# Optimization experiments

Measured on AMD Instinct MI355X. Metric: run time of the kernel, lower is better.

The kernel has to match this reference:

```python
import jax, jax.numpy as jnp
import numpy as np

IN, H, B = 1024, 1024, 8192


def _uniform(key, shape, stdv):
    return jax.random.uniform(key, shape, jnp.float32, -stdv, stdv)


def setup_inputs() -> dict:
    key = jax.random.key(0)
    ks = jax.random.split(key, 20)
    stdv = 1.0 / np.sqrt(H)
    inp = {
        "x": jax.random.normal(ks[0], (B, IN), jnp.float32),
        "h": jax.random.normal(ks[1], (B, H), jnp.float32),
        "c": jax.random.normal(ks[2], (B, H), jnp.float32),
        # fused input->gates weight [IN, 4H] (gate order: I, F, G, O) and bias [4H]
        "Wi": _uniform(ks[3], (IN, 4 * H), stdv),
        "bi": _uniform(ks[4], (4 * H,), stdv),
        # fused hidden->gates weight [H, 4H] and bias [4H]
        "Wh": _uniform(ks[5], (H, 4 * H), stdv),
        "bh": _uniform(ks[6], (4 * H,), stdv),
    }
    return inp


def reference(x, h, c, Wi, bi, Wh, bh):
    # Two fused GEMMs replacing the 8 separate nn.Linear calls (same math).
    gates = x @ Wi + bi + h @ Wh + bh  # [B, 4H]
    gI, gF, gG, gO = jnp.split(gates, 4, axis=-1)
    I = jax.nn.sigmoid(gI)
    F = jax.nn.sigmoid(gF)
    G = jnp.tanh(gG)   # nlF = Tanh
    O = jax.nn.sigmoid(gO)
    c_ = F * c + I * G
    h_ = O * jnp.tanh(c_)  # nlF2 = Tanh
    return (h_, c_)
```

## Files before the change

kernel.cpp:

```cpp
#include <hip/hip_runtime.h>
#include <stdint.h>

#define IN_DIM 1024
#define H_DIM  1024
#define BATCH  8192
#define KDIM   2048
#define NDIM   4096
#define BM     256
#define BN     256
#define BK     64
#define NT     (KDIM / BK)

typedef __bf16 bf16x8 __attribute__((ext_vector_type(8)));
typedef float  f32x4  __attribute__((ext_vector_type(4)));
typedef unsigned int u32;

static __device__ __forceinline__ unsigned short f2bf(float f) {
  u32 u = __builtin_bit_cast(u32, f);
  u += 0x7FFFu + ((u >> 16) & 1u);
  return (unsigned short)(u >> 16);
}

static __device__ __forceinline__ float sigm(float x) {
  return 1.0f / (1.0f + __expf(-x));
}
static __device__ __forceinline__ float tanh_fast(float x) {
  float e = __expf(-2.0f * fabsf(x));
  float t = (1.0f - e) / (1.0f + e);
  return copysignf(t, x);
}

__global__ void conv_a(const float* __restrict__ x, const float* __restrict__ h,
                       unsigned short* __restrict__ A) {
  const int total = BATCH * KDIM / 4;
  for (int i = blockIdx.x * blockDim.x + threadIdx.x; i < total;
       i += gridDim.x * blockDim.x) {
    int b = i >> 9;
    int k = (i & 511) << 2;
    const float* src = (k < IN_DIM) ? (x + (size_t)b * IN_DIM + k)
                                    : (h + (size_t)b * H_DIM + (k - IN_DIM));
    float4 v = *reinterpret_cast<const float4*>(src);
    ushort4 o;
    o.x = f2bf(v.x); o.y = f2bf(v.y); o.z = f2bf(v.z); o.w = f2bf(v.w);
    *reinterpret_cast<ushort4*>(A + (size_t)b * KDIM + k) = o;
  }
}

__global__ void conv_b(const float* __restrict__ Wi, const float* __restrict__ Wh,
                       unsigned short* __restrict__ Bt) {
  __shared__ float tile[32][33];
  int k0 = blockIdx.x * 32;
  int c0 = blockIdx.y * 32;
  int tx = threadIdx.x;
  int ty = threadIdx.y;
  const float* src = (k0 < IN_DIM) ? (Wi + (size_t)k0 * NDIM)
                                   : (Wh + (size_t)(k0 - IN_DIM) * NDIM);
  for (int i = 0; i < 4; i++) {
    int r = ty + 8 * i;
    tile[r][tx] = src[(size_t)r * NDIM + c0 + tx];
  }
  __syncthreads();
  int g = c0 >> 10;
  int ubase = c0 & 1023;
  for (int i = 0; i < 4; i++) {
    int cc = ty + 8 * i;
    int u = ubase + cc;
    int j = ((u >> 4) << 6) + (g << 4) + (u & 15);
    Bt[(size_t)j * KDIM + k0 + tx] = f2bf(tile[tx][cc]);
  }
}

__global__ void conv_bias(const float* __restrict__ bi, const float* __restrict__ bh,
                          float* __restrict__ bias) {
  int j = blockIdx.x * blockDim.x + threadIdx.x;
  if (j < NDIM) {
    int u = ((j >> 6) << 4) + (j & 15);
    int g = (j >> 4) & 3;
    int c = (g << 10) + u;
    bias[j] = bi[c] + bh[c];
  }
}

static __device__ __forceinline__ void gload_lds16(const void* g, void* l) {
  __builtin_amdgcn_global_load_lds(
      (const __attribute__((address_space(1))) u32*)g,
      (__attribute__((address_space(3))) u32*)l, 16, 0, 0);
}

#define MFMA __builtin_amdgcn_mfma_f32_16x16x32_bf16
#define SGB  __builtin_amdgcn_sched_group_barrier

__launch_bounds__(512, 2)
__global__ void lstm_gemm(const unsigned short* __restrict__ A,
                          const unsigned short* __restrict__ Bt,
                          const float* __restrict__ bias,
                          const float* __restrict__ Cin,
                          float* __restrict__ Hout,
                          float* __restrict__ Cout) {
  __shared__ __align__(16) char smem[131072];

  const int t  = threadIdx.x;
  const int l  = t & 63;
  const int w  = t >> 6;
  const int lane16 = l & 15;
  const int kg = l >> 4;
  const int wr = w >> 2;
  const int wc = w & 3;

  int bid = blockIdx.x;
  int swz = (bid & 7) * 64 + (bid >> 3);
  int brow = (swz >> 4) * BM;
  int bcol = (swz & 15) * BN;

  int slot0 = w * 128 + l, slot1 = slot0 + 64;
  int rih0 = slot0 >> 3, rih1 = slot1 >> 3;
  int c0 = (slot0 & 7) ^ (rih0 & 7), c1 = (slot1 & 7) ^ (rih1 & 7);

  const unsigned short* a0q0 = A + (size_t)(brow + (rih0 >> 6) * 128 + (rih0 & 63)) * KDIM + c0 * 8;
  const unsigned short* a0q1 = A + (size_t)(brow + (rih1 >> 6) * 128 + (rih1 & 63)) * KDIM + c1 * 8;
  const unsigned short* a1q0 = a0q0 + 131072;
  const unsigned short* a1q1 = a0q1 + 131072;
  const unsigned short* b0q0 = Bt + (size_t)(bcol + (rih0 >> 5) * 64 + (rih0 & 31)) * KDIM + c0 * 8;
  const unsigned short* b0q1 = Bt + (size_t)(bcol + (rih1 >> 5) * 64 + (rih1 & 31)) * KDIM + c1 * 8;
  const unsigned short* b1q0 = b0q0 + 65536;
  const unsigned short* b1q1 = b0q1 + 65536;

#define GL(gp, loff) gload_lds16((gp), smem + (loff) + w * 2048 + l * 16)

  const int msk = (lane16 & 7) << 4;
  char* vA0 = smem + wr * 8192 + lane16 * 128 + ((kg * 16) ^ msk);
  char* vA1 = smem + wr * 8192 + lane16 * 128 + ((64 + kg * 16) ^ msk);
  char* vB0 = smem + 65536 + wc * 4096 + lane16 * 128 + ((kg * 16) ^ msk);
  char* vB1 = smem + 65536 + wc * 4096 + lane16 * 128 + ((64 + kg * 16) ^ msk);

  f32x4 acc[8][4];
#pragma unroll
  for (int m = 0; m < 8; m++)
#pragma unroll
    for (int n = 0; n < 4; n++) acc[m][n] = (f32x4){0.f, 0.f, 0.f, 0.f};

  GL(a0q0, 0);                 GL(a0q1, 1024);
  GL(b0q0, 65536);             GL(b0q1, 65536 + 1024);
  GL(a1q0, 16384);             GL(a1q1, 16384 + 1024);
  GL(b1q0, 65536 + 16384);     GL(b1q1, 65536 + 16384 + 1024);
  GL(a0q0 + 64, 32768);        GL(a0q1 + 64, 32768 + 1024);
  GL(b0q0 + 64, 65536 + 32768);GL(b0q1 + 64, 65536 + 32768 + 1024);
  asm volatile("s_waitcnt vmcnt(4)" ::: "memory");
  __builtin_amdgcn_s_barrier();
  __builtin_amdgcn_sched_barrier(0);
  GL(a1q0 + 64, 32768 + 16384); GL(a1q1 + 64, 32768 + 16384 + 1024);

  bf16x8 afrA[4][2], afrB[4][2], bfr[4][2];

#pragma unroll
  for (int mm = 0; mm < 4; mm++) {
    afrA[mm][0] = *(const bf16x8*)(vA0 + mm * 2048);
    afrA[mm][1] = *(const bf16x8*)(vA1 + mm * 2048);
  }
#pragma unroll
  for (int nn = 0; nn < 2; nn++) {
    bfr[nn][0] = *(const bf16x8*)(vB0 + nn * 2048);
    bfr[nn][1] = *(const bf16x8*)(vB1 + nn * 2048);
  }
  a0q0 += 128; a0q1 += 128; a1q0 += 128; a1q1 += 128;
  b0q0 += 128; b0q1 += 128; b1q0 += 64;  b1q1 += 64;

#define BODY(P)                                                              \
  {                                                                          \
    \
    GL(b1q0, 65536 + ((P)^1)*32768 + 16384);                                 \
    GL(b1q1, 65536 + ((P)^1)*32768 + 16384 + 1024);                          \
                           \
    __builtin_amdgcn_s_setprio(1);                                           \
    _Pragma("unroll") for (int nn = 2; nn < 4; nn++) {                       \
      bfr[nn][0] = *(const bf16x8*)(vB0 + (P)*32768 + 16384 + (nn-2)*2048);  \
      bfr[nn][1] = *(const bf16x8*)(vB1 + (P)*32768 + 16384 + (nn-2)*2048);  \
    }                                                                        \
    _Pragma("unroll") for (int mm = 0; mm < 4; mm++)                         \
      _Pragma("unroll") for (int nn = 0; nn < 2; nn++) {                     \
        acc[mm][nn] = MFMA(afrA[mm][0], bfr[nn][0], acc[mm][nn], 0, 0, 0);   \
        acc[mm][nn] = MFMA(afrA[mm][1], bfr[nn][1], acc[mm][nn], 0, 0, 0);   \
      }                                                                      \
    SGB(0x100, 1, 0); SGB(0x8, 4, 0);                                        \
    SGB(0x100, 1, 0); SGB(0x8, 4, 0);                                        \
    SGB(0x100, 1, 0); SGB(0x8, 4, 0);                                        \
    SGB(0x100, 1, 0); SGB(0x8, 4, 0);                                        \
    __builtin_amdgcn_s_setprio(0);                                           \
    __builtin_amdgcn_s_barrier();                                 \
    __builtin_amdgcn_sched_barrier(0);                                       \
         \
    GL(a0q0, (P)*32768);                                                     \
    GL(a0q1, (P)*32768 + 1024);                                              \
                       \
    __builtin_amdgcn_s_setprio(1);                                           \
    _Pragma("unroll") for (int mm = 0; mm < 4; mm++) {                       \
      afrB[mm][0] = *(const bf16x8*)(vA0 + (P)*32768 + 16384 + mm*2048);     \
      afrB[mm][1] = *(const bf16x8*)(vA1 + (P)*32768 + 16384 + mm*2048);     \
    }                                                                        \
    _Pragma("unroll") for (int mm = 0; mm < 4; mm++)                         \
      _Pragma("unroll") for (int nn = 2; nn < 4; nn++) {                     \
        acc[mm][nn] = MFMA(afrA[mm][0], bfr[nn][0], acc[mm][nn], 0, 0, 0);   \
        acc[mm][nn] = MFMA(afrA[mm][1], bfr[nn][1], acc[mm][nn], 0, 0, 0);   \
      }                                                                      \
    SGB(0x100, 2, 0); SGB(0x8, 4, 0);                                        \
    SGB(0x100, 2, 0); SGB(0x8, 4, 0);                                        \
    SGB(0x100, 2, 0); SGB(0x8, 4, 0);                                        \
    SGB(0x100, 2, 0); SGB(0x8, 4, 0);                                        \
    __builtin_amdgcn_s_setprio(0);                                           \
        \
    GL(b0q0, 65536 + (P)*32768);                                             \
    GL(b0q1, 65536 + (P)*32768 + 1024);                                      \
                            \
    __builtin_amdgcn_s_setprio(1);                                           \
    _Pragma("unroll") for (int mm = 0; mm < 4; mm++)                         \
      _Pragma("unroll") for (int nn = 0; nn < 2; nn++) {                     \
        acc[4+mm][nn] = MFMA(afrB[mm][0], bfr[nn][0], acc[4+mm][nn], 0, 0, 0);\
        acc[4+mm][nn] = MFMA(afrB[mm][1], bfr[nn][1], acc[4+mm][nn], 0, 0, 0);\
      }                                                                      \
    __builtin_amdgcn_s_setprio(0);                                           \
    \
    asm volatile("s_waitcnt vmcnt(4)" ::: "memory");                         \
    __builtin_amdgcn_s_barrier();                                 \
    __builtin_amdgcn_sched_barrier(0);                                       \
           \
    GL(a1q0, (P)*32768 + 16384);                                             \
    GL(a1q1, (P)*32768 + 16384 + 1024);                                      \
             \
    __builtin_amdgcn_s_setprio(1);                                           \
    _Pragma("unroll") for (int mm = 0; mm < 4; mm++) {                       \
      afrA[mm][0] = *(const bf16x8*)(vA0 + ((P)^1)*32768 + mm*2048);         \
      afrA[mm][1] = *(const bf16x8*)(vA1 + ((P)^1)*32768 + mm*2048);         \
    }                                                                        \
    _Pragma("unroll") for (int nn = 0; nn < 2; nn++) {                       \
      bfr[nn][0] = *(const bf16x8*)(vB0 + ((P)^1)*32768 + nn*2048);          \
      bfr[nn][1] = *(const bf16x8*)(vB1 + ((P)^1)*32768 + nn*2048);          \
    }                                                                        \
    _Pragma("unroll") for (int mm = 0; mm < 4; mm++)                         \
      _Pragma("unroll") for (int nn = 2; nn < 4; nn++) {                     \
        acc[4+mm][nn] = MFMA(afrB[mm][0], bfr[nn][0], acc[4+mm][nn], 0, 0, 0);\
        acc[4+mm][nn] = MFMA(afrB[mm][1], bfr[nn][1], acc[4+mm][nn], 0, 0, 0);\
      }                                                                      \
    SGB(0x100, 3, 0); SGB(0x8, 4, 0);                                        \
    SGB(0x100, 3, 0); SGB(0x8, 4, 0);                                        \
    SGB(0x100, 3, 0); SGB(0x8, 4, 0);                                        \
    SGB(0x100, 3, 0); SGB(0x8, 4, 0);                                        \
    __builtin_amdgcn_s_setprio(0);                                           \
    a0q0 += 64; a0q1 += 64; a1q0 += 64; a1q1 += 64;                          \
    b0q0 += 64; b0q1 += 64; b1q0 += 64; b1q1 += 64;                          \
  }

  for (int it = 0; it < NT / 2; ++it) {
    BODY(0)
    BODY(1)
  }
#undef BODY
#undef GL

  asm volatile("s_waitcnt vmcnt(0)" ::: "memory");

  const int U = (bcol >> 2) + wc * 16 + lane16;
  const float* cinp = Cin + (size_t)(brow + wr * 128 + kg * 4) * H_DIM + U;
  float cin[32];
#pragma unroll
  for (int m = 0; m < 8; m++)
#pragma unroll
    for (int r = 0; r < 4; r++)
      cin[m * 4 + r] = cinp[(size_t)(m * 16 + r) * H_DIM];
  float bv[4];
#pragma unroll
  for (int nn = 0; nn < 4; nn++)
    bv[nn] = bias[bcol + wc * 64 + nn * 16 + lane16];

  float* hp = Hout + (size_t)(brow + wr * 128 + kg * 4) * H_DIM + U;
  float* cp = Cout + (size_t)(brow + wr * 128 + kg * 4) * H_DIM + U;
#pragma unroll
  for (int m = 0; m < 8; m++)
#pragma unroll
    for (int r = 0; r < 4; r++) {
      float Ig = sigm(acc[m][0][r] + bv[0]);
      float Fg = sigm(acc[m][1][r] + bv[1]);
      float Gg = tanh_fast(acc[m][2][r] + bv[2]);
      float Og = sigm(acc[m][3][r] + bv[3]);
      float cn = Fg * cin[m * 4 + r] + Ig * Gg;
      size_t off = (size_t)(m * 16 + r) * H_DIM;
      hp[off] = Og * tanh_fast(cn);
      cp[off] = cn;
    }
}

extern "C" void kernel_launch(void* const* d_in, const int* in_sizes, int n_in,
                              void* d_out, int out_size, void* d_ws, size_t ws_size,
                              hipStream_t stream) {
  const float* x  = (const float*)d_in[0];
  const float* h  = (const float*)d_in[1];
  const float* c  = (const float*)d_in[2];
  const float* Wi = (const float*)d_in[3];
  const float* bi = (const float*)d_in[4];
  const float* Wh = (const float*)d_in[5];
  const float* bh = (const float*)d_in[6];

  float* out  = (float*)d_out;
  float* Hout = out;
  float* Cout = out + (size_t)BATCH * H_DIM;

  unsigned short* Abf = (unsigned short*)d_ws;
  unsigned short* Btb = (unsigned short*)((char*)d_ws + 33554432);
  float*          bsf = (float*)((char*)d_ws + 50331648);

  conv_a<<<2048, 256, 0, stream>>>(x, h, Abf);
  conv_b<<<dim3(64, 128), dim3(32, 8), 0, stream>>>(Wi, Wh, Btb);
  conv_bias<<<16, 256, 0, stream>>>(bi, bh, bsf);
  lstm_gemm<<<512, 512, 0, stream>>>(Abf, Btb, bsf, c, Hout, Cout);
}
```

Baseline: 155.7 us.

## Switch GEMM inner loop to 32x32x16 bf16 MFMA with shuffle-based LSTM epilogue

Replaces the 16x16x32 MFMA tiling with 32x32x16 MFMAs. Each wave now holds 4x2 tiles of 16-float accumulators, and the LDS fragment addressing and swizzle are rebuilt to match. The larger MFMA shape is meant to cut LDS fragment reads and instruction count per unit of math. The epilogue is reorganised so that each 32-column tile pairs the I/F and G/O gates across lane halves. The I*G product moves between lanes via a cross-lane shuffle, and only the upper half of the lanes write outputs, which leaves half the lanes idle in the epilogue and duplicates some sigmoid work.

```diff
diff --git a/kernel.cpp b/kernel.cpp
--- a/kernel.cpp
+++ b/kernel.cpp
@@ -12,7 +12,7 @@
 #define NT     (KDIM / BK)
 
 typedef __bf16 bf16x8 __attribute__((ext_vector_type(8)));
-typedef float  f32x4  __attribute__((ext_vector_type(4)));
+typedef float  f32x16 __attribute__((ext_vector_type(16)));
 typedef unsigned int u32;
 
 static __device__ __forceinline__ unsigned short f2bf(float f) {
@@ -87,7 +87,7 @@
       (__attribute__((address_space(3))) u32*)l, 16, 0, 0);
 }
 
-#define MFMA __builtin_amdgcn_mfma_f32_16x16x32_bf16
+#define MFMA32 __builtin_amdgcn_mfma_f32_32x32x16_bf16
 #define SGB  __builtin_amdgcn_sched_group_barrier
 
 __launch_bounds__(512, 2)
@@ -102,8 +102,7 @@
   const int t  = threadIdx.x;
   const int l  = t & 63;
   const int w  = t >> 6;
-  const int lane16 = l & 15;
-  const int kg = l >> 4;
+  const int l31 = l & 31;
   const int wr = w >> 2;
   const int wc = w & 3;
 
@@ -127,17 +126,23 @@
 
 #define GL(gp, loff) gload_lds16((gp), smem + (loff) + w * 2048 + l * 16)
 
-  const int msk = (lane16 & 7) << 4;
-  char* vA0 = smem + wr * 8192 + lane16 * 128 + ((kg * 16) ^ msk);
-  char* vA1 = smem + wr * 8192 + lane16 * 128 + ((64 + kg * 16) ^ msk);
-  char* vB0 = smem + 65536 + wc * 4096 + lane16 * 128 + ((kg * 16) ^ msk);
-  char* vB1 = smem + 65536 + wc * 4096 + lane16 * 128 + ((64 + kg * 16) ^ msk);
-
-  f32x4 acc[8][4];
-#pragma unroll
-  for (int m = 0; m < 8; m++)
-#pragma unroll
-    for (int n = 0; n < 4; n++) acc[m][n] = (f32x4){0.f, 0.f, 0.f, 0.f};
+  const int q4 = ((l >> 5) ^ (l & 7)) << 4;
+  char* vA_s[4];
+  char* vB_s[4];
+#pragma unroll
+  for (int s = 0; s < 4; s++) {
+    int off = ((s << 5) ^ q4);
+    vA_s[s] = smem + (wr * 64 + l31) * 128 + off;
+    vB_s[s] = smem + 65536 + (wc * 32 + l31) * 128 + off;
+  }
+
+  f32x16 acc[4][2];
+#pragma unroll
+  for (int m = 0; m < 4; m++)
+#pragma unroll
+    for (int n = 0; n < 2; n++)
+#pragma unroll
+      for (int r = 0; r < 16; r++) acc[m][n][r] = 0.f;
 
   GL(a0q0, 0);                 GL(a0q1, 1024);
   GL(b0q0, 65536);             GL(b0q1, 65536 + 1024);
@@ -150,100 +155,87 @@
   __builtin_amdgcn_sched_barrier(0);
   GL(a1q0 + 64, 32768 + 16384); GL(a1q1 + 64, 32768 + 16384 + 1024);
 
-  bf16x8 afrA[4][2], afrB[4][2], bfr[4][2];
-
-#pragma unroll
-  for (int mm = 0; mm < 4; mm++) {
-    afrA[mm][0] = *(const bf16x8*)(vA0 + mm * 2048);
-    afrA[mm][1] = *(const bf16x8*)(vA1 + mm * 2048);
-  }
-#pragma unroll
-  for (int nn = 0; nn < 2; nn++) {
-    bfr[nn][0] = *(const bf16x8*)(vB0 + nn * 2048);
-    bfr[nn][1] = *(const bf16x8*)(vB1 + nn * 2048);
+  bf16x8 afrA[2][4], afrB[2][4], bfrN0[4], bfrN1[4];
+
+#pragma unroll
+  for (int s = 0; s < 4; s++) {
+    afrA[0][s] = *(const bf16x8*)(vA_s[s]);
+    afrA[1][s] = *(const bf16x8*)(vA_s[s] + 4096);
+    bfrN0[s]   = *(const bf16x8*)(vB_s[s]);
   }
   a0q0 += 128; a0q1 += 128; a1q0 += 128; a1q1 += 128;
   b0q0 += 128; b0q1 += 128; b1q0 += 64;  b1q1 += 64;
 
 #define BODY(P)                                                              \
   {                                                                          \
-    \
+                                             \
     GL(b1q0, 65536 + ((P)^1)*32768 + 16384);                                 \
     GL(b1q1, 65536 + ((P)^1)*32768 + 16384 + 1024);                          \
-                           \
+                 \
     __builtin_amdgcn_s_setprio(1);                                           \
-    _Pragma("unroll") for (int nn = 2; nn < 4; nn++) {                       \
-      bfr[nn][0] = *(const bf16x8*)(vB0 + (P)*32768 + 16384 + (nn-2)*2048);  \
-      bfr[nn][1] = *(const bf16x8*)(vB1 + (P)*32768 + 16384 + (nn-2)*2048);  \
-    }                                                                        \
-    _Pragma("unroll") for (int mm = 0; mm < 4; mm++)                         \
-      _Pragma("unroll") for (int nn = 0; nn < 2; nn++) {                     \
-        acc[mm][nn] = MFMA(afrA[mm][0], bfr[nn][0], acc[mm][nn], 0, 0, 0);   \
-        acc[mm][nn] = MFMA(afrA[mm][1], bfr[nn][1], acc[mm][nn], 0, 0, 0);   \
-      }                                                                      \
-    SGB(0x100, 1, 0); SGB(0x8, 4, 0);                                        \
-    SGB(0x100, 1, 0); SGB(0x8, 4, 0);                                        \
-    SGB(0x100, 1, 0); SGB(0x8, 4, 0);                                        \
-    SGB(0x100, 1, 0); SGB(0x8, 4, 0);                                        \
+    _Pragma("unroll") for (int s = 0; s < 4; s++)                            \
+      bfrN1[s] = *(const bf16x8*)(vB_s[s] + (P)*32768 + 16384);              \
+    _Pragma("unroll") for (int s = 0; s < 4; s++)                            \
+      _Pragma("unroll") for (int mt = 0; mt < 2; mt++)                       \
+        acc[mt][0] = MFMA32(afrA[mt][s], bfrN0[s], acc[mt][0], 0, 0, 0);     \
+    SGB(0x100, 1, 0); SGB(0x8, 2, 0);                                        \
+    SGB(0x100, 1, 0); SGB(0x8, 2, 0);                                        \
+    SGB(0x100, 1, 0); SGB(0x8, 2, 0);                                        \
+    SGB(0x100, 1, 0); SGB(0x8, 2, 0);                                        \
     __builtin_amdgcn_s_setprio(0);                                           \
     __builtin_amdgcn_s_barrier();                                 \
     __builtin_amdgcn_sched_barrier(0);                                       \
-         \
+                                             \
     GL(a0q0, (P)*32768);                                                     \
     GL(a0q1, (P)*32768 + 1024);                                              \
-                       \
+     \
     __builtin_amdgcn_s_setprio(1);                                           \
-    _Pragma("unroll") for (int mm = 0; mm < 4; mm++) {                       \
-      afrB[mm][0] = *(const bf16x8*)(vA0 + (P)*32768 + 16384 + mm*2048);     \
-      afrB[mm][1] = *(const bf16x8*)(vA1 + (P)*32768 + 16384 + mm*2048);     \
+    _Pragma("unroll") for (int s = 0; s < 4; s++) {                          \
+      afrB[0][s] = *(const bf16x8*)(vA_s[s] + (P)*32768 + 16384);            \
+      afrB[1][s] = *(const bf16x8*)(vA_s[s] + (P)*32768 + 16384 + 4096);     \
     }                                                                        \
-    _Pragma("unroll") for (int mm = 0; mm < 4; mm++)                         \
-      _Pragma("unroll") for (int nn = 2; nn < 4; nn++) {                     \
-        acc[mm][nn] = MFMA(afrA[mm][0], bfr[nn][0], acc[mm][nn], 0, 0, 0);   \
-        acc[mm][nn] = MFMA(afrA[mm][1], bfr[nn][1], acc[mm][nn], 0, 0, 0);   \
-      }                                                                      \
-    SGB(0x100, 2, 0); SGB(0x8, 4, 0);                                        \
-    SGB(0x100, 2, 0); SGB(0x8, 4, 0);                                        \
-    SGB(0x100, 2, 0); SGB(0x8, 4, 0);                                        \
-    SGB(0x100, 2, 0); SGB(0x8, 4, 0);                                        \
+    _Pragma("unroll") for (int s = 0; s < 4; s++)                            \
+      _Pragma("unroll") for (int mt = 0; mt < 2; mt++)                       \
+        acc[mt][1] = MFMA32(afrA[mt][s], bfrN1[s], acc[mt][1], 0, 0, 0);     \
+    SGB(0x100, 1, 0); SGB(0x8, 1, 0);                                        \
+    SGB(0x100, 1, 0); SGB(0x8, 1, 0);                                        \
+    SGB(0x100, 1, 0); SGB(0x8, 1, 0);                                        \
+    SGB(0x100, 1, 0); SGB(0x8, 1, 0);                                        \
+    SGB(0x100, 1, 0); SGB(0x8, 1, 0);                                        \
+    SGB(0x100, 1, 0); SGB(0x8, 1, 0);                                        \
+    SGB(0x100, 1, 0); SGB(0x8, 1, 0);                                        \
+    SGB(0x100, 1, 0); SGB(0x8, 1, 0);                                        \
     __builtin_amdgcn_s_setprio(0);                                           \
-        \
+                                             \
     GL(b0q0, 65536 + (P)*32768);                                             \
     GL(b0q1, 65536 + (P)*32768 + 1024);                                      \
-                            \
+                  \
     __builtin_amdgcn_s_setprio(1);                                           \
-    _Pragma("unroll") for (int mm = 0; mm < 4; mm++)                         \
-      _Pragma("unroll") for (int nn = 0; nn < 2; nn++) {                     \
-        acc[4+mm][nn] = MFMA(afrB[mm][0], bfr[nn][0], acc[4+mm][nn], 0, 0, 0);\
-        acc[4+mm][nn] = MFMA(afrB[mm][1], bfr[nn][1], acc[4+mm][nn], 0, 0, 0);\
-      }                                                                      \
+    _Pragma("unroll") for (int s = 0; s < 4; s++)                            \
+      _Pragma("unroll") for (int mt = 0; mt < 2; mt++)                       \
+        acc[2+mt][0] = MFMA32(afrB[mt][s], bfrN0[s], acc[2+mt][0], 0, 0, 0); \
     __builtin_amdgcn_s_setprio(0);                                           \
-    \
+         \
     asm volatile("s_waitcnt vmcnt(4)" ::: "memory");                         \
     __builtin_amdgcn_s_barrier();                                 \
     __builtin_amdgcn_sched_barrier(0);                                       \
-           \
+                                             \
     GL(a1q0, (P)*32768 + 16384);                                             \
     GL(a1q1, (P)*32768 + 16384 + 1024);                                      \
-             \
+        \
     __builtin_amdgcn_s_setprio(1);                                           \
-    _Pragma("unroll") for (int mm = 0; mm < 4; mm++) {                       \
-      afrA[mm][0] = *(const bf16x8*)(vA0 + ((P)^1)*32768 + mm*2048);         \
-      afrA[mm][1] = *(const bf16x8*)(vA1 + ((P)^1)*32768 + mm*2048);         \
+    _Pragma("unroll") for (int s = 0; s < 4; s++) {                          \
+      afrA[0][s] = *(const bf16x8*)(vA_s[s] + ((P)^1)*32768);                \
+      afrA[1][s] = *(const bf16x8*)(vA_s[s] + ((P)^1)*32768 + 4096);         \
+      bfrN0[s]   = *(const bf16x8*)(vB_s[s] + ((P)^1)*32768);                \
     }                                                                        \
-    _Pragma("unroll") for (int nn = 0; nn < 2; nn++) {                       \
-      bfr[nn][0] = *(const bf16x8*)(vB0 + ((P)^1)*32768 + nn*2048);          \
-      bfr[nn][1] = *(const bf16x8*)(vB1 + ((P)^1)*32768 + nn*2048);          \
-    }                                                                        \
-    _Pragma("unroll") for (int mm = 0; mm < 4; mm++)                         \
-      _Pragma("unroll") for (int nn = 2; nn < 4; nn++) {                     \
-        acc[4+mm][nn] = MFMA(afrB[mm][0], bfr[nn][0], acc[4+mm][nn], 0, 0, 0);\
-        acc[4+mm][nn] = MFMA(afrB[mm][1], bfr[nn][1], acc[4+mm][nn], 0, 0, 0);\
-      }                                                                      \
-    SGB(0x100, 3, 0); SGB(0x8, 4, 0);                                        \
-    SGB(0x100, 3, 0); SGB(0x8, 4, 0);                                        \
-    SGB(0x100, 3, 0); SGB(0x8, 4, 0);                                        \
-    SGB(0x100, 3, 0); SGB(0x8, 4, 0);                                        \
+    _Pragma("unroll") for (int s = 0; s < 4; s++)                            \
+      _Pragma("unroll") for (int mt = 0; mt < 2; mt++)                       \
+        acc[2+mt][1] = MFMA32(afrB[mt][s], bfrN1[s], acc[2+mt][1], 0, 0, 0); \
+    SGB(0x100, 3, 0); SGB(0x8, 2, 0);                                        \
+    SGB(0x100, 3, 0); SGB(0x8, 2, 0);                                        \
+    SGB(0x100, 3, 0); SGB(0x8, 2, 0);                                        \
+    SGB(0x100, 3, 0); SGB(0x8, 2, 0);                                        \
     __builtin_amdgcn_s_setprio(0);                                           \
     a0q0 += 64; a0q1 += 64; a1q0 += 64; a1q1 += 64;                          \
     b0q0 += 64; b0q1 += 64; b1q0 += 64; b1q1 += 64;                          \
@@ -258,33 +250,29 @@
 
   asm volatile("s_waitcnt vmcnt(0)" ::: "memory");
 
-  const int U = (bcol >> 2) + wc * 16 + lane16;
-  const float* cinp = Cin + (size_t)(brow + wr * 128 + kg * 4) * H_DIM + U;
-  float cin[32];
-#pragma unroll
-  for (int m = 0; m < 8; m++)
-#pragma unroll
-    for (int r = 0; r < 4; r++)
-      cin[m * 4 + r] = cinp[(size_t)(m * 16 + r) * H_DIM];
-  float bv[4];
-#pragma unroll
-  for (int nn = 0; nn < 4; nn++)
-    bv[nn] = bias[bcol + wc * 64 + nn * 16 + lane16];
-
-  float* hp = Hout + (size_t)(brow + wr * 128 + kg * 4) * H_DIM + U;
-  float* cp = Cout + (size_t)(brow + wr * 128 + kg * 4) * H_DIM + U;
-#pragma unroll
-  for (int m = 0; m < 8; m++)
-#pragma unroll
-    for (int r = 0; r < 4; r++) {
-      float Ig = sigm(acc[m][0][r] + bv[0]);
-      float Fg = sigm(acc[m][1][r] + bv[1]);
-      float Gg = tanh_fast(acc[m][2][r] + bv[2]);
-      float Og = sigm(acc[m][3][r] + bv[3]);
-      float cn = Fg * cin[m * 4 + r] + Ig * Gg;
-      size_t off = (size_t)(m * 16 + r) * H_DIM;
-      hp[off] = Og * tanh_fast(cn);
-      cp[off] = cn;
+  const float bv0 = bias[bcol + 64 * wc + l31];
+  const float bv1 = bias[bcol + 64 * wc + 32 + l31];
+  const bool hi = (l & 16) != 0;
+  const int U = (bcol >> 2) + wc * 16 + (l & 15);
+  const int rbase = brow + wr * 128 + 4 * (l >> 5);
+
+#pragma unroll
+  for (int mt = 0; mt < 4; mt++)
+#pragma unroll
+    for (int r = 0; r < 16; r++) {
+      float g0 = acc[mt][0][r] + bv0;
+      float g1 = acc[mt][1][r] + bv1;
+      float IG = sigm(g0) * tanh_fast(g1);
+      float P  = __shfl_xor(IG, 16);
+      if (hi) {
+        int row = rbase + mt * 32 + (r & 3) + 8 * (r >> 2);
+        size_t idx = (size_t)row * H_DIM + U;
+        float F = sigm(g0);
+        float O = sigm(g1);
+        float cn = F * Cin[idx] + P;
+        Hout[idx] = O * tanh_fast(cn);
+        Cout[idx] = cn;
+      }
     }
 }
 
```

Measured after the change: 204.1 us. 1.31x slower.
